# Kernel tuning notes

Hardware: AMD Instinct MI355X
Metric: run time of the kernel (lower is better)

## Reference

```python
import jax, jax.numpy as jnp
import numpy as np

H = 8          # n_heads
D_HEAD = 64    # head_dim; scores scaled by sqrt(D_HEAD)


def setup_inputs() -> dict:
    key = jax.random.key(0)
    ks = jax.random.split(key, 9)
    B, S, Dm = 8, 1024, 512
    return {
        "input_Q": jax.random.normal(ks[0], (B, S, Dm), jnp.float32),
        "input_K": jax.random.normal(ks[1], (B, S, Dm), jnp.float32),
        "input_V": jax.random.normal(ks[2], (B, S, Dm), jnp.float32),
        "attn_mask": jax.random.randint(ks[3], (B, S, S), 0, 2).astype(bool),
        "edge_encoding": jax.random.normal(ks[4], (B, S, S), jnp.float32),
        "W_Q": jax.random.normal(ks[5], (Dm, Dm), jnp.float32) / np.sqrt(Dm),
        "W_K": jax.random.normal(ks[6], (Dm, Dm), jnp.float32) / np.sqrt(Dm),
        "W_V": jax.random.normal(ks[7], (Dm, Dm), jnp.float32) / np.sqrt(Dm),
        "W_fc": jax.random.normal(ks[8], (Dm, Dm), jnp.float32) / np.sqrt(Dm),
    }


def reference(input_Q, input_K, input_V, attn_mask, edge_encoding, W_Q, W_K, W_V, W_fc):
    B, S, Dm = input_Q.shape
    # project and split heads: [B, H, S, d_head]
    def heads(x, W):
        return (x @ W).reshape(B, S, H, D_HEAD).transpose(0, 2, 1, 3)
    Q = heads(input_Q, W_Q)
    K = heads(input_K, W_K)
    V = heads(input_V, W_V)
    scores = jnp.einsum("bhqd,bhkd->bhqk", Q, K) / np.sqrt(D_HEAD)
    scores = scores + edge_encoding[:, None, :, :]
    scores = jnp.where(attn_mask[:, None, :, :], jnp.float32(-1e9), scores)
    attn = jax.nn.softmax(scores, axis=-1)
    context = jnp.einsum("bhqk,bhkd->bhqd", attn, V)
    context = context.transpose(0, 2, 1, 3).reshape(B, S, Dm)
    output = context @ W_fc
    scores_avg = scores.sum(axis=1) / H  # [B, S, S]
    return output, scores_avg
```

## Files before the change

kernel.cpp:

```cpp
#include <hip/hip_runtime.h>
#include <math.h>

#define B_ 8
#define S_ 1024
#define DM 512
#define H_ 8
#define DH 64

typedef _Float16 h4 __attribute__((ext_vector_type(4)));
typedef _Float16 h8 __attribute__((ext_vector_type(8)));
typedef float f4 __attribute__((ext_vector_type(4)));

#define MFMA16(a, b, c) __builtin_amdgcn_mfma_f32_16x16x32_f16(a, b, c, 0, 0, 0)

__global__ __launch_bounds__(256) void cast_x(
    const float* __restrict__ x0, const float* __restrict__ x1,
    const float* __restrict__ x2, _Float16* __restrict__ y0,
    _Float16* __restrict__ y1, _Float16* __restrict__ y2) {
  const float* x = (blockIdx.y == 0) ? x0 : (blockIdx.y == 1) ? x1 : x2;
  _Float16* y = (blockIdx.y == 0) ? y0 : (blockIdx.y == 1) ? y1 : y2;
  size_t i = (size_t)blockIdx.x * 1024 + (size_t)threadIdx.x * 4;
  float4 v = *(const float4*)(x + i);
  h4 hv = {(_Float16)v.x, (_Float16)v.y, (_Float16)v.z, (_Float16)v.w};
  *(h4*)(y + i) = hv;
}

__global__ __launch_bounds__(256) void cast_w(
    const float* __restrict__ w0, const float* __restrict__ w1,
    const float* __restrict__ w2, const float* __restrict__ w3,
    _Float16* __restrict__ t0, _Float16* __restrict__ t1,
    _Float16* __restrict__ t2, _Float16* __restrict__ t3) {
  const float* W;
  _Float16* T;
  switch (blockIdx.z) {
    case 0: W = w0; T = t0; break;
    case 1: W = w1; T = t1; break;
    case 2: W = w2; T = t2; break;
    default: W = w3; T = t3; break;
  }
  __shared__ _Float16 ts[64][72];
  const int t = threadIdx.x;
  const int r = t >> 2, c0 = (t & 3) * 16;
  const int n0 = blockIdx.x * 64, k0 = blockIdx.y * 64;
#pragma unroll
  for (int i = 0; i < 4; i++) {
    float4 v = *(const float4*)&W[(size_t)(k0 + r) * 512 + n0 + c0 + i * 4];
    h4 hv = {(_Float16)v.x, (_Float16)v.y, (_Float16)v.z, (_Float16)v.w};
    *(h4*)&ts[r][c0 + i * 4] = hv;
  }
  __syncthreads();
  alignas(16) _Float16 outv[16];
#pragma unroll
  for (int i = 0; i < 16; i++) outv[i] = ts[c0 + i][r];
  *(uint4*)&T[(size_t)(n0 + r) * 512 + k0 + c0] = *(uint4*)&outv[0];
  *(uint4*)&T[(size_t)(n0 + r) * 512 + k0 + c0 + 8] = *(uint4*)&outv[8];
}

__global__ __launch_bounds__(256) void transpose_v(
    const _Float16* __restrict__ Vh, _Float16* __restrict__ Vth) {
  const int bh = blockIdx.y, b = bh >> 3, h = bh & 7;
  const int s0 = blockIdx.x * 64;
  __shared__ _Float16 ts[64][72];
  const int t = threadIdx.x;
  const int r = t >> 2, c0 = (t & 3) * 16;
  const size_t src = ((size_t)b * S_ + s0 + r) * DM + h * DH + c0;
  *(uint4*)&ts[r][c0] = *(const uint4*)&Vh[src];
  *(uint4*)&ts[r][c0 + 8] = *(const uint4*)&Vh[src + 8];
  __syncthreads();
  alignas(16) _Float16 outv[16];
#pragma unroll
  for (int i = 0; i < 16; i++) outv[i] = ts[c0 + i][r];
  const size_t dst = ((size_t)bh * 64 + r) * S_ + s0 + c0;
  *(uint4*)&Vth[dst] = *(uint4*)&outv[0];
  *(uint4*)&Vth[dst + 8] = *(uint4*)&outv[8];
}

template <bool F32OUT>
__global__ __launch_bounds__(256) void gemm_h(
    const _Float16* __restrict__ A, const _Float16* __restrict__ Bt,
    void* __restrict__ Cout, int M, int N, int K) {
  __shared__ _Float16 As[64][72], Bs[64][72];
  const int t = threadIdx.x, lane = t & 63, w = t >> 6;
  const int quad = lane >> 4, l16 = lane & 15;
  const int row0 = blockIdx.y * 64, col0 = blockIdx.x * 64;
  f4 acc[4] = {};
  for (int k0 = 0; k0 < K; k0 += 64) {
#pragma unroll
    for (int i = 0; i < 2; i++) {
      int c = t + i * 256;
      int r = c >> 3, cs = (c & 7) * 8;
      *(uint4*)&As[r][cs] = *(const uint4*)&A[(size_t)(row0 + r) * K + k0 + cs];
      *(uint4*)&Bs[r][cs] = *(const uint4*)&Bt[(size_t)(col0 + r) * K + k0 + cs];
    }
    __syncthreads();
    h8 a0 = *(h8*)&As[w * 16 + l16][quad * 8];
    h8 a1 = *(h8*)&As[w * 16 + l16][32 + quad * 8];
#pragma unroll
    for (int n = 0; n < 4; n++) {
      h8 b0 = *(h8*)&Bs[n * 16 + l16][quad * 8];
      h8 b1 = *(h8*)&Bs[n * 16 + l16][32 + quad * 8];
      acc[n] = MFMA16(a0, b0, acc[n]);
      acc[n] = MFMA16(a1, b1, acc[n]);
    }
    __syncthreads();
  }
#pragma unroll
  for (int n = 0; n < 4; n++)
#pragma unroll
    for (int reg = 0; reg < 4; reg++) {
      size_t row = row0 + w * 16 + quad * 4 + reg;
      size_t col = col0 + n * 16 + l16;
      if (F32OUT)
        ((float*)Cout)[row * N + col] = acc[n][reg];
      else
        ((_Float16*)Cout)[row * N + col] = (_Float16)acc[n][reg];
    }
}

__global__ __launch_bounds__(256) void scores_mfma(
    const _Float16* __restrict__ Qh, const _Float16* __restrict__ Kh,
    const int* __restrict__ mask, const float* __restrict__ edge,
    float* __restrict__ out1) {
  const int b = blockIdx.z;
  const int i0 = blockIdx.y * 64, j0 = blockIdx.x * 64;
  const _Float16* A = Qh + (size_t)b * S_ * DM;
  const _Float16* Bt = Kh + (size_t)b * S_ * DM;
  __shared__ _Float16 As[64][72], Bs[64][72];
  const int t = threadIdx.x, lane = t & 63, w = t >> 6;
  const int quad = lane >> 4, l16 = lane & 15;
  f4 acc[4] = {};
  for (int k0 = 0; k0 < DM; k0 += 64) {
#pragma unroll
    for (int i = 0; i < 2; i++) {
      int c = t + i * 256;
      int r = c >> 3, cs = (c & 7) * 8;
      *(uint4*)&As[r][cs] = *(const uint4*)&A[(size_t)(i0 + r) * DM + k0 + cs];
      *(uint4*)&Bs[r][cs] = *(const uint4*)&Bt[(size_t)(j0 + r) * DM + k0 + cs];
    }
    __syncthreads();
    h8 a0 = *(h8*)&As[w * 16 + l16][quad * 8];
    h8 a1 = *(h8*)&As[w * 16 + l16][32 + quad * 8];
#pragma unroll
    for (int n = 0; n < 4; n++) {
      h8 b0 = *(h8*)&Bs[n * 16 + l16][quad * 8];
      h8 b1 = *(h8*)&Bs[n * 16 + l16][32 + quad * 8];
      acc[n] = MFMA16(a0, b0, acc[n]);
      acc[n] = MFMA16(a1, b1, acc[n]);
    }
    __syncthreads();
  }
#pragma unroll
  for (int n = 0; n < 4; n++)
#pragma unroll
    for (int reg = 0; reg < 4; reg++) {
      size_t gi = i0 + w * 16 + quad * 4 + reg;
      size_t gj = j0 + n * 16 + l16;
      size_t idx = ((size_t)b * S_ + gi) * S_ + gj;
      float v = acc[n][reg] * (1.0f / 64.0f) + edge[idx];
      out1[idx] = mask[idx] ? -1e9f : v;
    }
}

__global__ __launch_bounds__(256, 2) void flash_mfma(
    const _Float16* __restrict__ Qh, const _Float16* __restrict__ Kh,
    const _Float16* __restrict__ Vth, const int* __restrict__ mask,
    const float* __restrict__ edge, _Float16* __restrict__ ctxh) {
  __shared__ _Float16 Qs[64][72], Ks[64][72], Vt[64][72], Ps[64][72];
  const int t = threadIdx.x, lane = t & 63, w = t >> 6;
  const int quad = lane >> 4, l16 = lane & 15;
  const int bh = blockIdx.y, b = bh >> 3, h = bh & 7;
  const int q0 = blockIdx.x * 64;
  const size_t bS = (size_t)b * S_;
  const int rqb = w * 16 + quad * 4;

#pragma unroll
  for (int i = 0; i < 2; i++) {
    int c = t + i * 256;
    int r = c >> 3, cs = (c & 7) * 8;
    *(uint4*)&Qs[r][cs] = *(const uint4*)&Qh[(bS + q0 + r) * DM + h * DH + cs];
  }
  __syncthreads();
  h8 aq0 = *(h8*)&Qs[w * 16 + l16][quad * 8];
  h8 aq1 = *(h8*)&Qs[w * 16 + l16][32 + quad * 8];

  f4 acco[4] = {};
  float m_run[4], l_run[4];
#pragma unroll
  for (int r = 0; r < 4; r++) {
    m_run[r] = -INFINITY;
    l_run[r] = 0.f;
  }

  for (int kb = 0; kb < S_; kb += 64) {
    __syncthreads();
#pragma unroll
    for (int i = 0; i < 2; i++) {
      int c = t + i * 256;
      int r = c >> 3, cs = (c & 7) * 8;
      *(uint4*)&Ks[r][cs] =
          *(const uint4*)&Kh[(bS + kb + r) * DM + h * DH + cs];
      *(uint4*)&Vt[r][cs] =
          *(const uint4*)&Vth[((size_t)bh * 64 + r) * S_ + kb + cs];
    }
    __syncthreads();
    f4 accs[4] = {};
#pragma unroll
    for (int n = 0; n < 4; n++) {
      h8 b0 = *(h8*)&Ks[n * 16 + l16][quad * 8];
      h8 b1 = *(h8*)&Ks[n * 16 + l16][32 + quad * 8];
      accs[n] = MFMA16(aq0, b0, accs[n]);
      accs[n] = MFMA16(aq1, b1, accs[n]);
    }
    float sv[4][4];
#pragma unroll
    for (int n = 0; n < 4; n++)
#pragma unroll
      for (int reg = 0; reg < 4; reg++) {
        size_t eidx = (bS + q0 + rqb + reg) * (size_t)S_ + kb + n * 16 + l16;
        float s = accs[n][reg] * 0.125f + edge[eidx];
        sv[n][reg] = mask[eidx] ? -1e9f : s;
      }
#pragma unroll
    for (int reg = 0; reg < 4; reg++) {
      float mx = fmaxf(fmaxf(sv[0][reg], sv[1][reg]),
                       fmaxf(sv[2][reg], sv[3][reg]));
#pragma unroll
      for (int off = 1; off < 16; off <<= 1)
        mx = fmaxf(mx, __shfl_xor(mx, off, 16));
      float mnew = fmaxf(m_run[reg], mx);
      float alpha = __expf(m_run[reg] - mnew);
      m_run[reg] = mnew;
      float psum = 0.f;
#pragma unroll
      for (int n = 0; n < 4; n++) {
        float p = __expf(sv[n][reg] - mnew);
        sv[n][reg] = p;
        psum += p;
      }
#pragma unroll
      for (int off = 1; off < 16; off <<= 1) psum += __shfl_xor(psum, off, 16);
      l_run[reg] = l_run[reg] * alpha + psum;
#pragma unroll
      for (int n = 0; n < 4; n++) acco[n][reg] *= alpha;
    }
#pragma unroll
    for (int n = 0; n < 4; n++)
#pragma unroll
      for (int reg = 0; reg < 4; reg++)
        Ps[rqb + reg][n * 16 + l16] = (_Float16)sv[n][reg];
    h8 ap0 = *(h8*)&Ps[w * 16 + l16][quad * 8];
    h8 ap1 = *(h8*)&Ps[w * 16 + l16][32 + quad * 8];
#pragma unroll
    for (int n = 0; n < 4; n++) {
      h8 bv0 = *(h8*)&Vt[n * 16 + l16][quad * 8];
      h8 bv1 = *(h8*)&Vt[n * 16 + l16][32 + quad * 8];
      acco[n] = MFMA16(ap0, bv0, acco[n]);
      acco[n] = MFMA16(ap1, bv1, acco[n]);
    }
  }
#pragma unroll
  for (int n = 0; n < 4; n++)
#pragma unroll
    for (int reg = 0; reg < 4; reg++) {
      float o = acco[n][reg] / l_run[reg];
      ctxh[(bS + q0 + rqb + reg) * DM + h * DH + n * 16 + l16] = (_Float16)o;
    }
}

extern "C" void kernel_launch(void* const* d_in, const int* in_sizes, int n_in,
                              void* d_out, int out_size, void* d_ws,
                              size_t ws_size, hipStream_t stream) {
  const float* Xq = (const float*)d_in[0];
  const float* Xk = (const float*)d_in[1];
  const float* Xv = (const float*)d_in[2];
  const int* mask = (const int*)d_in[3];
  const float* edge = (const float*)d_in[4];
  const float* Wq = (const float*)d_in[5];
  const float* Wk = (const float*)d_in[6];
  const float* Wv = (const float*)d_in[7];
  const float* Wfc = (const float*)d_in[8];

  float* out0 = (float*)d_out;
  float* out1 = out0 + (size_t)B_ * S_ * DM;

  const size_t NE = (size_t)B_ * S_ * DM;
  char* ws = (char*)d_ws;
  _Float16* Qh = (_Float16*)ws;
  _Float16* Kh = Qh + NE;
  _Float16* Vh = Kh + NE;
  _Float16* Xhq = Vh + NE;
  _Float16* Xhk = Xhq + NE;
  _Float16* Xhv = Xhk + NE;
  _Float16* Wt = Xhv + NE;
  _Float16* Wtq = Wt, *Wtk = Wt + 512 * 512, *Wtv = Wt + 2 * 512 * 512,
            *Wtf = Wt + 3 * 512 * 512;
  _Float16* ctxh = Xhq;
  _Float16* Vth = Xhk;

  dim3 blk(256);
  cast_x<<<dim3(4096, 3), blk, 0, stream>>>(Xq, Xk, Xv, Xhq, Xhk, Xhv);
  cast_w<<<dim3(8, 8, 4), blk, 0, stream>>>(Wq, Wk, Wv, Wfc, Wtq, Wtk, Wtv,
                                            Wtf);
  dim3 gp(DM / 64, (B_ * S_) / 64);
  gemm_h<false><<<gp, blk, 0, stream>>>(Xhq, Wtq, Qh, B_ * S_, DM, DM);
  gemm_h<false><<<gp, blk, 0, stream>>>(Xhk, Wtk, Kh, B_ * S_, DM, DM);
  gemm_h<false><<<gp, blk, 0, stream>>>(Xhv, Wtv, Vh, B_ * S_, DM, DM);
  transpose_v<<<dim3(16, 64), blk, 0, stream>>>(Vh, Vth);
  flash_mfma<<<dim3(16, 64), blk, 0, stream>>>(Qh, Kh, Vth, mask, edge, ctxh);
  gemm_h<true><<<gp, blk, 0, stream>>>(ctxh, Wtf, out0, B_ * S_, DM, DM);
  scores_mfma<<<dim3(16, 16, 8), blk, 0, stream>>>(Qh, Kh, mask, edge, out1);
}
```

Before: 424.7 us.

## Precompute fp16 masked edge bias, retile GEMMs to 128x128 with register prefetch

The scores kernel now runs before the flash kernel and also writes a combined fp16 bias tensor, holding the edge value or -65504 where masked. The flash kernel then reads this single half-precision array instead of the fp32 edge and int32 mask, which cuts its per-head memory traffic across all eight heads. Both the GEMM and scores kernels move to 128x128 tiles with a 4x4 MFMA block per warp, and global loads for the next K/V or K-slice are prefetched into registers. The costs are extra register pressure, dropping the flash kernel's occupancy hint, an extra S×S fp16 write, and fp16 rounding of the edge values inside the softmax.

```diff
diff --git a/kernel.cpp b/kernel.cpp
--- a/kernel.cpp
+++ b/kernel.cpp
@@ -79,109 +79,170 @@
 __global__ __launch_bounds__(256) void gemm_h(
     const _Float16* __restrict__ A, const _Float16* __restrict__ Bt,
     void* __restrict__ Cout, int M, int N, int K) {
-  __shared__ _Float16 As[64][72], Bs[64][72];
+  __shared__ _Float16 As[128][72], Bs[128][72];
   const int t = threadIdx.x, lane = t & 63, w = t >> 6;
   const int quad = lane >> 4, l16 = lane & 15;
-  const int row0 = blockIdx.y * 64, col0 = blockIdx.x * 64;
-  f4 acc[4] = {};
+  const int row0 = blockIdx.y * 128, col0 = blockIdx.x * 128;
+  const int wm = (w & 1) * 64, wn = (w >> 1) * 64;
+  const int gr = t >> 3, gc = (t & 7) * 8;
+  f4 acc[4][4] = {};
+  uint4 pa[4], pb[4];
+#pragma unroll
+  for (int i = 0; i < 4; i++) {
+    pa[i] = *(const uint4*)&A[(size_t)(row0 + gr + 32 * i) * K + gc];
+    pb[i] = *(const uint4*)&Bt[(size_t)(col0 + gr + 32 * i) * K + gc];
+  }
   for (int k0 = 0; k0 < K; k0 += 64) {
-#pragma unroll
-    for (int i = 0; i < 2; i++) {
-      int c = t + i * 256;
-      int r = c >> 3, cs = (c & 7) * 8;
-      *(uint4*)&As[r][cs] = *(const uint4*)&A[(size_t)(row0 + r) * K + k0 + cs];
-      *(uint4*)&Bs[r][cs] = *(const uint4*)&Bt[(size_t)(col0 + r) * K + k0 + cs];
-    }
-    __syncthreads();
-    h8 a0 = *(h8*)&As[w * 16 + l16][quad * 8];
-    h8 a1 = *(h8*)&As[w * 16 + l16][32 + quad * 8];
+    __syncthreads();
+#pragma unroll
+    for (int i = 0; i < 4; i++) {
+      *(uint4*)&As[gr + 32 * i][gc] = pa[i];
+      *(uint4*)&Bs[gr + 32 * i][gc] = pb[i];
+    }
+    __syncthreads();
+    if (k0 + 64 < K) {
+#pragma unroll
+      for (int i = 0; i < 4; i++) {
+        pa[i] = *(const uint4*)&A[(size_t)(row0 + gr + 32 * i) * K + k0 + 64 + gc];
+        pb[i] = *(const uint4*)&Bt[(size_t)(col0 + gr + 32 * i) * K + k0 + 64 + gc];
+      }
+    }
+    h8 af[4][2], bf[4][2];
+#pragma unroll
+    for (int m = 0; m < 4; m++) {
+      af[m][0] = *(h8*)&As[wm + m * 16 + l16][quad * 8];
+      af[m][1] = *(h8*)&As[wm + m * 16 + l16][32 + quad * 8];
+    }
 #pragma unroll
     for (int n = 0; n < 4; n++) {
-      h8 b0 = *(h8*)&Bs[n * 16 + l16][quad * 8];
-      h8 b1 = *(h8*)&Bs[n * 16 + l16][32 + quad * 8];
-      acc[n] = MFMA16(a0, b0, acc[n]);
-      acc[n] = MFMA16(a1, b1, acc[n]);
-    }
-    __syncthreads();
-  }
-#pragma unroll
-  for (int n = 0; n < 4; n++)
-#pragma unroll
-    for (int reg = 0; reg < 4; reg++) {
-      size_t row = row0 + w * 16 + quad * 4 + reg;
-      size_t col = col0 + n * 16 + l16;
-      if (F32OUT)
-        ((float*)Cout)[row * N + col] = acc[n][reg];
-      else
-        ((_Float16*)Cout)[row * N + col] = (_Float16)acc[n][reg];
-    }
+      bf[n][0] = *(h8*)&Bs[wn + n * 16 + l16][quad * 8];
+      bf[n][1] = *(h8*)&Bs[wn + n * 16 + l16][32 + quad * 8];
+    }
+#pragma unroll
+    for (int m = 0; m < 4; m++)
+#pragma unroll
+      for (int n = 0; n < 4; n++) {
+        acc[m][n] = MFMA16(af[m][0], bf[n][0], acc[m][n]);
+        acc[m][n] = MFMA16(af[m][1], bf[n][1], acc[m][n]);
+      }
+  }
+#pragma unroll
+  for (int m = 0; m < 4; m++)
+#pragma unroll
+    for (int n = 0; n < 4; n++)
+#pragma unroll
+      for (int reg = 0; reg < 4; reg++) {
+        size_t row = row0 + wm + m * 16 + quad * 4 + reg;
+        size_t col = col0 + wn + n * 16 + l16;
+        if (F32OUT)
+          ((float*)Cout)[row * N + col] = acc[m][n][reg];
+        else
+          ((_Float16*)Cout)[row * N + col] = (_Float16)acc[m][n][reg];
+      }
 }
 
 __global__ __launch_bounds__(256) void scores_mfma(
     const _Float16* __restrict__ Qh, const _Float16* __restrict__ Kh,
     const int* __restrict__ mask, const float* __restrict__ edge,
-    float* __restrict__ out1) {
+    float* __restrict__ out1, _Float16* __restrict__ Eh) {
   const int b = blockIdx.z;
-  const int i0 = blockIdx.y * 64, j0 = blockIdx.x * 64;
+  const int i0 = blockIdx.y * 128, j0 = blockIdx.x * 128;
   const _Float16* A = Qh + (size_t)b * S_ * DM;
   const _Float16* Bt = Kh + (size_t)b * S_ * DM;
-  __shared__ _Float16 As[64][72], Bs[64][72];
+  __shared__ _Float16 As[128][72], Bs[128][72];
   const int t = threadIdx.x, lane = t & 63, w = t >> 6;
   const int quad = lane >> 4, l16 = lane & 15;
-  f4 acc[4] = {};
+  const int wm = (w & 1) * 64, wn = (w >> 1) * 64;
+  const int gr = t >> 3, gc = (t & 7) * 8;
+  f4 acc[4][4] = {};
+  uint4 pa[4], pb[4];
+#pragma unroll
+  for (int i = 0; i < 4; i++) {
+    pa[i] = *(const uint4*)&A[(size_t)(i0 + gr + 32 * i) * DM + gc];
+    pb[i] = *(const uint4*)&Bt[(size_t)(j0 + gr + 32 * i) * DM + gc];
+  }
   for (int k0 = 0; k0 < DM; k0 += 64) {
-#pragma unroll
-    for (int i = 0; i < 2; i++) {
-      int c = t + i * 256;
-      int r = c >> 3, cs = (c & 7) * 8;
-      *(uint4*)&As[r][cs] = *(const uint4*)&A[(size_t)(i0 + r) * DM + k0 + cs];
-      *(uint4*)&Bs[r][cs] = *(const uint4*)&Bt[(size_t)(j0 + r) * DM + k0 + cs];
-    }
-    __syncthreads();
-    h8 a0 = *(h8*)&As[w * 16 + l16][quad * 8];
-    h8 a1 = *(h8*)&As[w * 16 + l16][32 + quad * 8];
+    __syncthreads();
+#pragma unroll
+    for (int i = 0; i < 4; i++) {
+      *(uint4*)&As[gr + 32 * i][gc] = pa[i];
+      *(uint4*)&Bs[gr + 32 * i][gc] = pb[i];
+    }
+    __syncthreads();
+    if (k0 + 64 < DM) {
+#pragma unroll
+      for (int i = 0; i < 4; i++) {
+        pa[i] = *(const uint4*)&A[(size_t)(i0 + gr + 32 * i) * DM + k0 + 64 + gc];
+        pb[i] = *(const uint4*)&Bt[(size_t)(j0 + gr + 32 * i) * DM + k0 + 64 + gc];
+      }
+    }
+    h8 af[4][2], bf[4][2];
+#pragma unroll
+    for (int m = 0; m < 4; m++) {
+      af[m][0] = *(h8*)&As[wm + m * 16 + l16][quad * 8];
+      af[m][1] = *(h8*)&As[wm + m * 16 + l16][32 + quad * 8];
+    }
 #pragma unroll
     for (int n = 0; n < 4; n++) {
-      h8 b0 = *(h8*)&Bs[n * 16 + l16][quad * 8];
-      h8 b1 = *(h8*)&Bs[n * 16 + l16][32 + quad * 8];
-      acc[n] = MFMA16(a0, b0, acc[n]);
-      acc[n] = MFMA16(a1, b1, acc[n]);
-    }
-    __syncthreads();
-  }
-#pragma unroll
-  for (int n = 0; n < 4; n++)
+      bf[n][0] = *(h8*)&Bs[wn + n * 16 + l16][quad * 8];
+      bf[n][1] = *(h8*)&Bs[wn + n * 16 + l16][32 + quad * 8];
+    }
+#pragma unroll
+    for (int m = 0; m < 4; m++)
+#pragma unroll
+      for (int n = 0; n < 4; n++) {
+        acc[m][n] = MFMA16(af[m][0], bf[n][0], acc[m][n]);
+        acc[m][n] = MFMA16(af[m][1], bf[n][1], acc[m][n]);
+      }
+  }
+#pragma unroll
+  for (int m = 0; m < 4; m++)
 #pragma unroll
     for (int reg = 0; reg < 4; reg++) {
-      size_t gi = i0 + w * 16 + quad * 4 + reg;
-      size_t gj = j0 + n * 16 + l16;
-      size_t idx = ((size_t)b * S_ + gi) * S_ + gj;
-      float v = acc[n][reg] * (1.0f / 64.0f) + edge[idx];
-      out1[idx] = mask[idx] ? -1e9f : v;
-    }
-}
-
-__global__ __launch_bounds__(256, 2) void flash_mfma(
+      size_t gi = i0 + wm + m * 16 + quad * 4 + reg;
+      size_t rowb = ((size_t)b * S_ + gi) * S_;
+#pragma unroll
+      for (int n = 0; n < 4; n++) {
+        size_t idx = rowb + j0 + wn + n * 16 + l16;
+        int mk = mask[idx];
+        float e = edge[idx];
+        out1[idx] = mk ? -1e9f : (acc[m][n][reg] * (1.0f / 64.0f) + e);
+        Eh[idx] = mk ? (_Float16)(-65504.0f) : (_Float16)e;
+      }
+    }
+}
+
+__global__ __launch_bounds__(256) void flash_mfma(
     const _Float16* __restrict__ Qh, const _Float16* __restrict__ Kh,
-    const _Float16* __restrict__ Vth, const int* __restrict__ mask,
-    const float* __restrict__ edge, _Float16* __restrict__ ctxh) {
-  __shared__ _Float16 Qs[64][72], Ks[64][72], Vt[64][72], Ps[64][72];
+    const _Float16* __restrict__ Vth, const _Float16* __restrict__ Eh,
+    _Float16* __restrict__ ctxh) {
+  __shared__ _Float16 Ps[64][72], Ks[64][72], Vt[64][72];
   const int t = threadIdx.x, lane = t & 63, w = t >> 6;
   const int quad = lane >> 4, l16 = lane & 15;
   const int bh = blockIdx.y, b = bh >> 3, h = bh & 7;
   const int q0 = blockIdx.x * 64;
   const size_t bS = (size_t)b * S_;
   const int rqb = w * 16 + quad * 4;
-
-#pragma unroll
-  for (int i = 0; i < 2; i++) {
-    int c = t + i * 256;
-    int r = c >> 3, cs = (c & 7) * 8;
-    *(uint4*)&Qs[r][cs] = *(const uint4*)&Qh[(bS + q0 + r) * DM + h * DH + cs];
-  }
+  const int sr = t >> 3, sc = (t & 7) * 8;
+
+  *(uint4*)&Ps[sr][sc] = *(const uint4*)&Qh[(bS + q0 + sr) * DM + h * DH + sc];
+  *(uint4*)&Ps[sr + 32][sc] =
+      *(const uint4*)&Qh[(bS + q0 + sr + 32) * DM + h * DH + sc];
   __syncthreads();
-  h8 aq0 = *(h8*)&Qs[w * 16 + l16][quad * 8];
-  h8 aq1 = *(h8*)&Qs[w * 16 + l16][32 + quad * 8];
+  h8 aq0 = *(h8*)&Ps[w * 16 + l16][quad * 8];
+  h8 aq1 = *(h8*)&Ps[w * 16 + l16][32 + quad * 8];
+
+  uint4 kv[4];
+  kv[0] = *(const uint4*)&Kh[(bS + sr) * DM + h * DH + sc];
+  kv[1] = *(const uint4*)&Kh[(bS + sr + 32) * DM + h * DH + sc];
+  kv[2] = *(const uint4*)&Vth[((size_t)bh * 64 + sr) * S_ + sc];
+  kv[3] = *(const uint4*)&Vth[((size_t)bh * 64 + sr + 32) * S_ + sc];
+  _Float16 evh[16];
+#pragma unroll
+  for (int n = 0; n < 4; n++)
+#pragma unroll
+    for (int reg = 0; reg < 4; reg++)
+      evh[n * 4 + reg] = Eh[(bS + q0 + rqb + reg) * S_ + n * 16 + l16];
 
   f4 acco[4] = {};
   float m_run[4], l_run[4];
@@ -193,16 +254,24 @@
 
   for (int kb = 0; kb < S_; kb += 64) {
     __syncthreads();
-#pragma unroll
-    for (int i = 0; i < 2; i++) {
-      int c = t + i * 256;
-      int r = c >> 3, cs = (c & 7) * 8;
-      *(uint4*)&Ks[r][cs] =
-          *(const uint4*)&Kh[(bS + kb + r) * DM + h * DH + cs];
-      *(uint4*)&Vt[r][cs] =
-          *(const uint4*)&Vth[((size_t)bh * 64 + r) * S_ + kb + cs];
-    }
-    __syncthreads();
+    *(uint4*)&Ks[sr][sc] = kv[0];
+    *(uint4*)&Ks[sr + 32][sc] = kv[1];
+    *(uint4*)&Vt[sr][sc] = kv[2];
+    *(uint4*)&Vt[sr + 32][sc] = kv[3];
+    __syncthreads();
+    const int kn = kb + 64;
+    _Float16 evn[16];
+    if (kn < S_) {
+      kv[0] = *(const uint4*)&Kh[(bS + kn + sr) * DM + h * DH + sc];
+      kv[1] = *(const uint4*)&Kh[(bS + kn + sr + 32) * DM + h * DH + sc];
+      kv[2] = *(const uint4*)&Vth[((size_t)bh * 64 + sr) * S_ + kn + sc];
+      kv[3] = *(const uint4*)&Vth[((size_t)bh * 64 + sr + 32) * S_ + kn + sc];
+#pragma unroll
+      for (int n = 0; n < 4; n++)
+#pragma unroll
+        for (int reg = 0; reg < 4; reg++)
+          evn[n * 4 + reg] = Eh[(bS + q0 + rqb + reg) * S_ + kn + n * 16 + l16];
+    }
     f4 accs[4] = {};
 #pragma unroll
     for (int n = 0; n < 4; n++) {
@@ -215,11 +284,8 @@
 #pragma unroll
     for (int n = 0; n < 4; n++)
 #pragma unroll
-      for (int reg = 0; reg < 4; reg++) {
-        size_t eidx = (bS + q0 + rqb + reg) * (size_t)S_ + kb + n * 16 + l16;
-        float s = accs[n][reg] * 0.125f + edge[eidx];
-        sv[n][reg] = mask[eidx] ? -1e9f : s;
-      }
+      for (int reg = 0; reg < 4; reg++)
+        sv[n][reg] = accs[n][reg] * 0.125f + (float)evh[n * 4 + reg];
 #pragma unroll
     for (int reg = 0; reg < 4; reg++) {
       float mx = fmaxf(fmaxf(sv[0][reg], sv[1][reg]),
@@ -256,6 +322,10 @@
       h8 bv1 = *(h8*)&Vt[n * 16 + l16][32 + quad * 8];
       acco[n] = MFMA16(ap0, bv0, acco[n]);
       acco[n] = MFMA16(ap1, bv1, acco[n]);
+    }
+    if (kn < S_) {
+#pragma unroll
+      for (int i = 0; i < 16; i++) evh[i] = evn[i];
     }
   }
 #pragma unroll
@@ -292,8 +362,9 @@
   _Float16* Xhk = Xhq + NE;
   _Float16* Xhv = Xhk + NE;
   _Float16* Wt = Xhv + NE;
-  _Float16* Wtq = Wt, *Wtk = Wt + 512 * 512, *Wtv = Wt + 2 * 512 * 512,
-            *Wtf = Wt + 3 * 512 * 512;
+  _Float16 *Wtq = Wt, *Wtk = Wt + 512 * 512, *Wtv = Wt + 2 * 512 * 512,
+           *Wtf = Wt + 3 * 512 * 512;
+  _Float16* Eh = Wt + 4 * 512 * 512;
   _Float16* ctxh = Xhq;
   _Float16* Vth = Xhk;
 
@@ -301,12 +372,12 @@
   cast_x<<<dim3(4096, 3), blk, 0, stream>>>(Xq, Xk, Xv, Xhq, Xhk, Xhv);
   cast_w<<<dim3(8, 8, 4), blk, 0, stream>>>(Wq, Wk, Wv, Wfc, Wtq, Wtk, Wtv,
                                             Wtf);
-  dim3 gp(DM / 64, (B_ * S_) / 64);
+  dim3 gp(DM / 128, (B_ * S_) / 128);
   gemm_h<false><<<gp, blk, 0, stream>>>(Xhq, Wtq, Qh, B_ * S_, DM, DM);
   gemm_h<false><<<gp, blk, 0, stream>>>(Xhk, Wtk, Kh, B_ * S_, DM, DM);
+  scores_mfma<<<dim3(8, 8, 8), blk, 0, stream>>>(Qh, Kh, mask, edge, out1, Eh);
   gemm_h<false><<<gp, blk, 0, stream>>>(Xhv, Wtv, Vh, B_ * S_, DM, DM);
   transpose_v<<<dim3(16, 64), blk, 0, stream>>>(Vh, Vth);
-  flash_mfma<<<dim3(16, 64), blk, 0, stream>>>(Qh, Kh, Vth, mask, edge, ctxh);
+  flash_mfma<<<dim3(16, 64), blk, 0, stream>>>(Qh, Kh, Vth, Eh, ctxh);
   gemm_h<true><<<gp, blk, 0, stream>>>(ctxh, Wtf, out0, B_ * S_, DM, DM);
-  scores_mfma<<<dim3(16, 16, 8), blk, 0, stream>>>(Qh, Kh, mask, edge, out1);
-}
+}
```

Result: no change. 425.8 us (+0.3%).
